# Kernel optimization log

Measured on AMD Instinct MI355X. Metric: run time of the kernel, lower is better.

The kernel has to match this reference:

```python
import jax, jax.numpy as jnp
import numpy as np

N = 100_000      # nodes
E = 1_600_000    # edges (avg degree 16)
IN = 512         # in_feats
HID = 4          # hidden_feats (forced equal to num_heads=4 by the mean(h,2) in forward)
H1 = 4           # heads in layer 1
OUT = 128        # out_feats
NEG_SLOPE = 0.2  # DGL GATConv leaky_relu default


def setup_inputs() -> dict:
    key = jax.random.key(0)
    ks = jax.random.split(key, 12)
    nfeats = jax.random.normal(ks[0], (N, IN), jnp.float32)
    efeats = jax.random.normal(ks[1], (E, 8), jnp.float32)  # unused by the module
    src = jax.random.randint(ks[2], (E,), 0, N, dtype=jnp.int32)
    dst = jax.random.randint(ks[3], (E,), 0, N, dtype=jnp.int32)
    # layer 1 params (in=IN, heads=H1, per-head out=HID)
    fc1_w = jax.random.normal(ks[4], (IN, H1 * HID), jnp.float32) / np.sqrt(IN)
    attn_l1 = jax.random.normal(ks[5], (H1, HID), jnp.float32) / np.sqrt(HID)
    attn_r1 = jax.random.normal(ks[6], (H1, HID), jnp.float32) / np.sqrt(HID)
    bias1 = jnp.zeros((H1 * HID,), jnp.float32)
    # layer 2 params (in=H1=4 after mean over feature dim, heads=1, out=OUT)
    fc2_w = jax.random.normal(ks[7], (HID, 1 * OUT), jnp.float32) / np.sqrt(HID)
    attn_l2 = jax.random.normal(ks[8], (1, OUT), jnp.float32) / np.sqrt(OUT)
    attn_r2 = jax.random.normal(ks[9], (1, OUT), jnp.float32) / np.sqrt(OUT)
    bias2 = jnp.zeros((OUT,), jnp.float32)
    return {"nfeats": nfeats, "efeats": efeats, "src": src, "dst": dst,
            "fc1_w": fc1_w, "attn_l1": attn_l1, "attn_r1": attn_r1, "bias1": bias1,
            "fc2_w": fc2_w, "attn_l2": attn_l2, "attn_r2": attn_r2, "bias2": bias2}


def gat_layer(x, src, dst, fc_w, attn_l, attn_r, bias, heads, d_out):
    # projection: (N, in) -> (N, H, D)
    h = (x @ fc_w).reshape(-1, heads, d_out)
    el = jnp.einsum('nhd,hd->nh', h, attn_l)   # (N, H)
    er = jnp.einsum('nhd,hd->nh', h, attn_r)
    e = jax.nn.leaky_relu(el[src] + er[dst], NEG_SLOPE)  # (E, H)
    # segment softmax over incoming edges of each dst node
    m = jax.lax.stop_gradient(jax.ops.segment_max(e, dst, num_segments=N))
    ex = jnp.exp(e - m[dst])
    denom = jax.ops.segment_sum(ex, dst, num_segments=N)
    alpha = ex / denom[dst]                    # (E, H)
    msg = alpha[:, :, None] * h[src]           # (E, H, D)
    rst = jax.ops.segment_sum(msg, dst, num_segments=N)  # (N, H, D)
    return rst + bias.reshape(1, heads, d_out)


def reference(nfeats, efeats, src, dst, fc1_w, attn_l1, attn_r1, bias1,
              fc2_w, attn_l2, attn_r2, bias2):
    h = gat_layer(nfeats, src, dst, fc1_w, attn_l1, attn_r1, bias1, H1, HID)  # (N,4,4)
    h = jnp.mean(h, axis=2)        # faithful to th.mean(h, 2): mean over per-head feat dim -> (N,4)
    h = jax.nn.relu(h)
    h = gat_layer(h, src, dst, fc2_w, attn_l2, attn_r2, bias2, 1, OUT)        # (N,1,OUT)
    return h.reshape(N, OUT)       # flatten(1)
```

## Files before the change

kernel.cpp:

```cpp
#include <hip/hip_runtime.h>
#include <math.h>

#define IN_F 512
#define OUTF 128
#define NEG_SLOPE 0.2f

typedef __attribute__((ext_vector_type(8))) short bf16x8;
typedef __attribute__((ext_vector_type(4))) float f32x4;

#define P1T 256
#define XP 136
#define NKS 16
#define BPSH 8192

#define NPB 128
#define NBMAX 784
#define EPB 4096
#define SRCMASK 0x1FFFF
#define CAP 2944

#define BP_BYTES (BPSH * 2)
#define XS_BYTES (4 * 16 * XP * 2)
#define SMEM_A   (BP_BYTES + XS_BYTES)

__device__ __forceinline__ unsigned pkbf(float a, float b) {
  unsigned ua = __float_as_uint(a); ua += 0x7FFF + ((ua >> 16) & 1);
  unsigned ub = __float_as_uint(b); ub += 0x7FFF + ((ub >> 16) & 1);
  return (ua >> 16) | (ub & 0xFFFF0000u);
}

__global__ void k_prep(const float* __restrict__ fc1, const float* __restrict__ al1,
                       const float* __restrict__ ar1, const float* __restrict__ fc2,
                       const float* __restrict__ al2, const float* __restrict__ ar2,
                       unsigned short* __restrict__ Bp,
                       float* __restrict__ w2al, float* __restrict__ w2ar,
                       int* __restrict__ bucketCursor) {
  __shared__ float wlds[IN_F * 12];
  int t = threadIdx.x;
  if (blockIdx.x == 0) {
    int k = t;
#pragma unroll
    for (int h = 0; h < 4; ++h) {
      float wl = 0.f, wr = 0.f, wb = 0.f;
#pragma unroll
      for (int j = 0; j < 4; ++j) {
        float wv = fc1[k * 16 + h * 4 + j];
        wl = fmaf(wv, al1[h * 4 + j], wl);
        wr = fmaf(wv, ar1[h * 4 + j], wr);
        wb += wv;
      }
      wlds[k * 12 + h] = wl;
      wlds[k * 12 + 4 + h] = wr;
      wlds[k * 12 + 8 + h] = 0.25f * wb;
    }
    __syncthreads();
    for (int item = t; item < NKS * 64; item += 512) {
      int s = item >> 6, l = item & 63;
      int col = l & 15;
      int kb = s * 32 + ((l >> 4) * 8);
      unsigned hi[4];
#pragma unroll
      for (int p = 0; p < 4; ++p) {
        float w0 = 0.f, w1 = 0.f;
        if (col < 12) {
          w0 = wlds[(kb + 2 * p) * 12 + col];
          w1 = wlds[(kb + 2 * p + 1) * 12 + col];
        }
        hi[p] = pkbf(w0, w1);
      }
      *(uint4*)&Bp[item * 8] = make_uint4(hi[0], hi[1], hi[2], hi[3]);
    }
  } else {
    if (t < 8) {
      int h = t >> 1;
      const float* a = (t & 1) ? ar2 : al2;
      float s = 0.f;
#pragma unroll 16
      for (int c = 0; c < OUTF; ++c) s += fc2[h * OUTF + c] * a[c];
      if (t & 1) w2ar[h] = s; else w2al[h] = s;
    }
    for (int i = t; i < NBMAX; i += 512) bucketCursor[i] = 0;
  }
}

__global__ __launch_bounds__(P1T) void k_A(
    const float* __restrict__ x, const unsigned short* __restrict__ Bp,
    float* __restrict__ pk1, float* __restrict__ er1, int n,
    const int* __restrict__ src, const int* __restrict__ dst,
    int* __restrict__ bucketCursor, unsigned* __restrict__ ep, int e,
    int projBlocks)
{
  __shared__ __align__(16) char smem[SMEM_A];
  const int t = threadIdx.x;

  if ((int)blockIdx.x < projBlocks) {
    const int lane = t & 63;
    const int wv = t >> 6;
    const bf16x8* Bfrag = (const bf16x8*)smem;
    short* xsw = (short*)(smem + BP_BYTES) + wv * (16 * XP);

    for (int i = t; i < NKS * 64; i += P1T)
      ((uint4*)smem)[i] = ((const uint4*)Bp)[i];
    __syncthreads();

    const int totalWaves = projBlocks * 4;
    const int rtMax = (n + 15) >> 4;
    for (int rt = blockIdx.x * 4 + wv; rt < rtMax; rt += totalWaves) {
      const int wrow = rt * 16;
      const float* __restrict__ xr = x + (size_t)wrow * IN_F;
      f32x4 acc = {0.f, 0.f, 0.f, 0.f};

      float4 st[8];
#pragma unroll
      for (int i = 0; i < 8; ++i) {
        int f = lane + i * 64;
        int r = f >> 5, c4 = (f & 31) * 4;
        st[i] = (wrow + r < n) ? *(const float4*)&xr[(size_t)r * IN_F + c4]
                               : make_float4(0.f, 0.f, 0.f, 0.f);
      }

      for (int kt = 0; kt < 4; ++kt) {
#pragma unroll
        for (int i = 0; i < 8; ++i) {
          int f = lane + i * 64;
          int r = f >> 5, c4 = (f & 31) * 4;
          uint2 pv; pv.x = pkbf(st[i].x, st[i].y); pv.y = pkbf(st[i].z, st[i].w);
          *(uint2*)&xsw[r * XP + c4] = pv;
        }
        if (kt < 3) {
          int kb = (kt + 1) * 128;
#pragma unroll
          for (int i = 0; i < 8; ++i) {
            int f = lane + i * 64;
            int r = f >> 5, c4 = (f & 31) * 4;
            st[i] = (wrow + r < n) ? *(const float4*)&xr[(size_t)r * IN_F + kb + c4]
                                   : make_float4(0.f, 0.f, 0.f, 0.f);
          }
        }
        asm volatile("s_waitcnt lgkmcnt(0)" ::: "memory");
        __builtin_amdgcn_sched_barrier(0);
#pragma unroll
        for (int ks = 0; ks < 4; ++ks) {
          bf16x8 a = *(const bf16x8*)&xsw[(lane & 15) * XP + ks * 32 + ((lane >> 4) * 8)];
          bf16x8 bh = Bfrag[(kt * 4 + ks) * 64 + lane];
          acc = __builtin_amdgcn_mfma_f32_16x16x32_bf16(a, bh, acc, 0, 0, 0);
        }
      }

      int col = lane & 15;
      int rbase = wrow + ((lane >> 4) * 4);
#pragma unroll
      for (int i = 0; i < 4; ++i) {
        int row = rbase + i;
        if (row < n) {
          float v = acc[i];
          if (col < 4)       pk1[(size_t)row * 8 + col] = v;
          else if (col < 8)  er1[(size_t)row * 4 + (col - 4)] = v;
          else if (col < 12) pk1[(size_t)row * 8 + 4 + (col - 8)] = v;
        }
      }
    }
  } else {
    int* hist = (int*)smem;
    int* base = hist + NBMAX;
    int* lcur = base + NBMAX;
    const int bb = blockIdx.x - projBlocks;
    for (int i = t; i < NBMAX; i += P1T) hist[i] = 0;
    __syncthreads();
    int blockBase = bb * EPB;
#pragma unroll
    for (int i = 0; i < EPB / P1T; ++i) {
      int idx = blockBase + t + i * P1T;
      if (idx < e) atomicAdd(&hist[dst[idx] >> 7], 1);
    }
    __syncthreads();
    for (int i = t; i < NBMAX; i += P1T) {
      if (hist[i] > 0) base[i] = atomicAdd(&bucketCursor[i], hist[i]);
      lcur[i] = 0;
    }
    __syncthreads();
#pragma unroll
    for (int i = 0; i < EPB / P1T; ++i) {
      int idx = blockBase + t + i * P1T;
      if (idx < e) {
        int d = dst[idx];
        int b = d >> 7;
        int off = base[b] + atomicAdd(&lcur[b], 1);
        if (off < CAP)
          ep[(size_t)b * CAP + off] = (unsigned)src[idx] | ((unsigned)(d & (NPB - 1)) << 17);
      }
    }
  }
}

__global__ __launch_bounds__(256) void k_B(
    const unsigned* __restrict__ ep, const int* __restrict__ bucketCursor,
    unsigned* __restrict__ ep2, int* __restrict__ nodeBeg, int* __restrict__ nodeEnd,
    const float* __restrict__ pk1, const float* __restrict__ er1,
    const float* __restrict__ bias1,
    const float* __restrict__ w2al, const float* __restrict__ w2ar,
    float* __restrict__ pk2, float* __restrict__ er2, int n)
{
  __shared__ int cnt[NPB];
  __shared__ int scn[NPB];
  __shared__ int cur[NPB];
  __shared__ unsigned lbuf[CAP];
  int t = threadIdx.x;
  int b = blockIdx.x;
  int nodeBase = b * NPB;
  int m = bucketCursor[b];
  if (m > CAP) m = CAP;
  const unsigned* __restrict__ in = ep + (size_t)b * CAP;
  if (t < NPB) cnt[t] = 0;
  __syncthreads();
  for (int j = t; j < m; j += 256) atomicAdd(&cnt[in[j] >> 17], 1);
  __syncthreads();
  if (t < NPB) scn[t] = cnt[t];
  __syncthreads();
  for (int off = 1; off < NPB; off <<= 1) {
    int v = (t < NPB && t >= off) ? scn[t - off] : 0;
    __syncthreads();
    if (t < NPB) scn[t] += v;
    __syncthreads();
  }
  if (t < NPB) {
    int excl = scn[t] - cnt[t];
    int node = nodeBase + t;
    if (node < n) {
      nodeBeg[node] = b * CAP + excl;
      nodeEnd[node] = b * CAP + excl + cnt[t];
    }
    cur[t] = excl;
  }
  __syncthreads();
  for (int j = t; j < m; j += 256) {
    unsigned p = in[j];
    int pos = atomicAdd(&cur[p >> 17], 1);
    lbuf[pos] = p & SRCMASK;
  }
  __syncthreads();
  for (int i = t; i < m; i += 256) ep2[(size_t)b * CAP + i] = lbuf[i];

#pragma unroll
  for (int half = 0; half < 2; ++half) {
    int w = t + half * 256;
    int i = w >> 2, h = w & 3;
    int node = nodeBase + i;
    bool active = node < n;
    float v = 0.f;
    if (active) {
      int beg = scn[i] - cnt[i], end = scn[i];
      float ern = er1[(size_t)node * 4 + h];
      float den = 0.f, num = 0.f;
      for (int j = beg; j < end; ++j) {
        int s = (int)lbuf[j];
        float el = pk1[(size_t)s * 8 + h];
        float hb = pk1[(size_t)s * 8 + 4 + h];
        float eh = el + ern;
        eh = (eh > 0.f) ? eh : NEG_SLOPE * eh;
        float wg = __expf(eh);
        den += wg;
        num = fmaf(wg, hb, num);
      }
      float mb = 0.25f * (bias1[h*4] + bias1[h*4+1] + bias1[h*4+2] + bias1[h*4+3]);
      v = (end > beg) ? num / den : 0.f;
      v += mb;
      v = (v > 0.f) ? v : 0.f;
    }
    float pl = v * w2al[h];
    float pr = v * w2ar[h];
    pl += __shfl_xor(pl, 1); pl += __shfl_xor(pl, 2);
    pr += __shfl_xor(pr, 1); pr += __shfl_xor(pr, 2);
    if (active) {
      pk2[(size_t)node * 8 + h] = v;
      if (h == 0) { pk2[(size_t)node * 8 + 4] = pl; er2[node] = pr; }
    }
  }
}

__global__ __launch_bounds__(256) void k_bagg2(
    const unsigned* __restrict__ ep2, const int* __restrict__ nodeBeg,
    const int* __restrict__ nodeEnd,
    const float* __restrict__ pk2, const float* __restrict__ er2,
    const float* __restrict__ w2, const float* __restrict__ bias2,
    float* __restrict__ out, int n)
{
  __shared__ float gacc[256 * 4];
  __shared__ float w2s[4 * OUTF];
  __shared__ float b2s[OUTF];
  int t = threadIdx.x;
  int nodeBase = blockIdx.x * 256;
  int nn = nodeBase + t;
  for (int i = t; i < 4 * OUTF; i += 256) w2s[i] = w2[i];
  if (t < OUTF) b2s[t] = bias2[t];
  float g0 = 0.f, g1 = 0.f, g2 = 0.f, g3 = 0.f;
  if (nn < n) {
    int beg = nodeBeg[nn], end = nodeEnd[nn];
    float ern = er2[nn];
    float den = 0.f;
    for (int j = beg; j < end; ++j) {
      int s = (int)ep2[j];
      const float* __restrict__ ps = &pk2[(size_t)s * 8];
      float4 hv = *(const float4*)ps;
      float e = ps[4] + ern;
      e = (e > 0.f) ? e : NEG_SLOPE * e;
      float w = __expf(e);
      den += w;
      g0 = fmaf(w, hv.x, g0); g1 = fmaf(w, hv.y, g1);
      g2 = fmaf(w, hv.z, g2); g3 = fmaf(w, hv.w, g3);
    }
    float inv = (end > beg) ? 1.0f / den : 0.f;
    g0 *= inv; g1 *= inv; g2 *= inv; g3 *= inv;
  }
  gacc[t * 4 + 0] = g0; gacc[t * 4 + 1] = g1;
  gacc[t * 4 + 2] = g2; gacc[t * 4 + 3] = g3;
  __syncthreads();
  for (int idx = t; idx < 256 * (OUTF / 2); idx += 256) {
    int i = idx >> 6;
    int node = nodeBase + i;
    if (node >= n) continue;
    int c = (idx & 63) * 2;
    float gx = gacc[i*4], gy = gacc[i*4+1], gz = gacc[i*4+2], gw = gacc[i*4+3];
    float2 o;
    o.x = gx*w2s[c]   + gy*w2s[OUTF+c]   + gz*w2s[2*OUTF+c]   + gw*w2s[3*OUTF+c]   + b2s[c];
    o.y = gx*w2s[c+1] + gy*w2s[OUTF+c+1] + gz*w2s[2*OUTF+c+1] + gw*w2s[3*OUTF+c+1] + b2s[c+1];
    *(float2*)&out[(size_t)node * OUTF + c] = o;
  }
}

extern "C" void kernel_launch(void* const* d_in, const int* in_sizes, int n_in,
                              void* d_out, int out_size, void* d_ws, size_t ws_size,
                              hipStream_t stream) {
  const float* nfeats = (const float*)d_in[0];
  const int*   srcp   = (const int*)d_in[2];
  const int*   dstp   = (const int*)d_in[3];
  const float* fc1    = (const float*)d_in[4];
  const float* al1    = (const float*)d_in[5];
  const float* ar1    = (const float*)d_in[6];
  const float* bias1  = (const float*)d_in[7];
  const float* fc2    = (const float*)d_in[8];
  const float* al2    = (const float*)d_in[9];
  const float* ar2    = (const float*)d_in[10];
  const float* bias2  = (const float*)d_in[11];

  const int N = in_sizes[0] / IN_F;
  const int E = in_sizes[2];
  const int NB = (N + NPB - 1) / NPB;

  float* ws   = (float*)d_ws;
  float* pk1  = ws;
  float* er1  = pk1 + (size_t)8 * N;
  float* pk2  = er1 + (size_t)4 * N;
  float* er2  = pk2 + (size_t)8 * N;
  float* w2al = er2 + N;
  float* w2ar = w2al + 4;
  unsigned short* Bp = (unsigned short*)(w2ar + 4);
  int* bucketCursor = (int*)(Bp + BPSH);
  int* nodeBeg      = bucketCursor + NBMAX;
  int* nodeEnd      = nodeBeg + N;
  unsigned* ep      = (unsigned*)(nodeEnd + N);
  unsigned* ep2     = ep + (size_t)NB * CAP;

  const int binBlocks = (E + EPB - 1) / EPB;
  const int projBlocks = 391;

  k_prep<<<2, 512, 0, stream>>>(fc1, al1, ar1, fc2, al2, ar2,
                                Bp, w2al, w2ar, bucketCursor);
  k_A<<<projBlocks + binBlocks, P1T, 0, stream>>>(nfeats, Bp, pk1, er1, N,
                                                  srcp, dstp, bucketCursor, ep, E,
                                                  projBlocks);
  k_B<<<NB, 256, 0, stream>>>(ep, bucketCursor, ep2, nodeBeg, nodeEnd,
                              pk1, er1, bias1, w2al, w2ar, pk2, er2, N);
  k_bagg2<<<(N + 255) / 256, 256, 0, stream>>>(ep2, nodeBeg, nodeEnd, pk2, er2,
                                               fc2, bias2, (float*)d_out, N);
}
```

Baseline: 136.6 us.

## Merge binning and projection into every block with dynamic tile scheduling

Kernel A used to give some blocks the projection and others the edge binning. Now every block first bins edges (if its index is below the binning block count) and then joins a work-stealing loop over 16-row projection tiles. Each wave grabs chunks of two tiles from a global atomic counter, which is reset in k_prep. Blocks grow to 512 threads and the grid is fixed at 768 blocks, with the aim of balancing load between the two phases and filling the GPU. The cost is global atomic contention and a doubled LDS footprint, which may cut occupancy.

Result: slower. 200.0 us (+46.4%).

```diff
diff --git a/kernel.cpp b/kernel.cpp
--- a/kernel.cpp
+++ b/kernel.cpp
@@ -8,10 +8,11 @@
 typedef __attribute__((ext_vector_type(8))) short bf16x8;
 typedef __attribute__((ext_vector_type(4))) float f32x4;
 
-#define P1T 256
+#define AT 512
 #define XP 136
 #define NKS 16
 #define BPSH 8192
+#define TCHUNK 2
 
 #define NPB 128
 #define NBMAX 784
@@ -20,7 +21,7 @@
 #define CAP 2944
 
 #define BP_BYTES (BPSH * 2)
-#define XS_BYTES (4 * 16 * XP * 2)
+#define XS_BYTES (8 * 16 * XP * 2)
 #define SMEM_A   (BP_BYTES + XS_BYTES)
 
 __device__ __forceinline__ unsigned pkbf(float a, float b) {
@@ -34,7 +35,7 @@
                        const float* __restrict__ al2, const float* __restrict__ ar2,
                        unsigned short* __restrict__ Bp,
                        float* __restrict__ w2al, float* __restrict__ w2ar,
-                       int* __restrict__ bucketCursor) {
+                       int* __restrict__ bucketCursor, int* __restrict__ tileCtr) {
   __shared__ float wlds[IN_F * 12];
   int t = threadIdx.x;
   if (blockIdx.x == 0) {
@@ -79,33 +80,70 @@
       for (int c = 0; c < OUTF; ++c) s += fc2[h * OUTF + c] * a[c];
       if (t & 1) w2ar[h] = s; else w2al[h] = s;
     }
+    if (t == 8) *tileCtr = 0;
     for (int i = t; i < NBMAX; i += 512) bucketCursor[i] = 0;
   }
 }
 
-__global__ __launch_bounds__(P1T) void k_A(
+__global__ __launch_bounds__(AT) void k_A(
     const float* __restrict__ x, const unsigned short* __restrict__ Bp,
     float* __restrict__ pk1, float* __restrict__ er1, int n,
     const int* __restrict__ src, const int* __restrict__ dst,
     int* __restrict__ bucketCursor, unsigned* __restrict__ ep, int e,
-    int projBlocks)
+    int* __restrict__ tileCtr, int bscatBlocks)
 {
   __shared__ __align__(16) char smem[SMEM_A];
   const int t = threadIdx.x;
 
-  if ((int)blockIdx.x < projBlocks) {
-    const int lane = t & 63;
-    const int wv = t >> 6;
-    const bf16x8* Bfrag = (const bf16x8*)smem;
-    short* xsw = (short*)(smem + BP_BYTES) + wv * (16 * XP);
-
-    for (int i = t; i < NKS * 64; i += P1T)
-      ((uint4*)smem)[i] = ((const uint4*)Bp)[i];
-    __syncthreads();
-
-    const int totalWaves = projBlocks * 4;
-    const int rtMax = (n + 15) >> 4;
-    for (int rt = blockIdx.x * 4 + wv; rt < rtMax; rt += totalWaves) {
+  if ((int)blockIdx.x < bscatBlocks) {
+    int* hist = (int*)smem;
+    int* base = hist + NBMAX;
+    int* lcur = base + NBMAX;
+    for (int i = t; i < NBMAX; i += AT) hist[i] = 0;
+    __syncthreads();
+    int blockBase = blockIdx.x * EPB;
+#pragma unroll
+    for (int i = 0; i < EPB / AT; ++i) {
+      int idx = blockBase + t + i * AT;
+      if (idx < e) atomicAdd(&hist[dst[idx] >> 7], 1);
+    }
+    __syncthreads();
+    for (int i = t; i < NBMAX; i += AT) {
+      if (hist[i] > 0) base[i] = atomicAdd(&bucketCursor[i], hist[i]);
+      lcur[i] = 0;
+    }
+    __syncthreads();
+#pragma unroll
+    for (int i = 0; i < EPB / AT; ++i) {
+      int idx = blockBase + t + i * AT;
+      if (idx < e) {
+        int d = dst[idx];
+        int b = d >> 7;
+        int off = base[b] + atomicAdd(&lcur[b], 1);
+        if (off < CAP)
+          ep[(size_t)b * CAP + off] = (unsigned)src[idx] | ((unsigned)(d & (NPB - 1)) << 17);
+      }
+    }
+    __syncthreads();
+  }
+
+  const int lane = t & 63;
+  const int wv = t >> 6;
+  const bf16x8* Bfrag = (const bf16x8*)smem;
+  short* xsw = (short*)(smem + BP_BYTES) + wv * (16 * XP);
+
+  for (int i = t; i < NKS * 64; i += AT)
+    ((uint4*)smem)[i] = ((const uint4*)Bp)[i];
+  __syncthreads();
+
+  const int rtMax = (n + 15) >> 4;
+  for (;;) {
+    int rt0;
+    if (lane == 0) rt0 = atomicAdd(tileCtr, TCHUNK);
+    rt0 = __shfl(rt0, 0);
+    if (rt0 >= rtMax) break;
+    int rtEnd = (rt0 + TCHUNK < rtMax) ? rt0 + TCHUNK : rtMax;
+    for (int rt = rt0; rt < rtEnd; ++rt) {
       const int wrow = rt * 16;
       const float* __restrict__ xr = x + (size_t)wrow * IN_F;
       f32x4 acc = {0.f, 0.f, 0.f, 0.f};
@@ -158,36 +196,6 @@
           else if (col < 8)  er1[(size_t)row * 4 + (col - 4)] = v;
           else if (col < 12) pk1[(size_t)row * 8 + 4 + (col - 8)] = v;
         }
-      }
-    }
-  } else {
-    int* hist = (int*)smem;
-    int* base = hist + NBMAX;
-    int* lcur = base + NBMAX;
-    const int bb = blockIdx.x - projBlocks;
-    for (int i = t; i < NBMAX; i += P1T) hist[i] = 0;
-    __syncthreads();
-    int blockBase = bb * EPB;
-#pragma unroll
-    for (int i = 0; i < EPB / P1T; ++i) {
-      int idx = blockBase + t + i * P1T;
-      if (idx < e) atomicAdd(&hist[dst[idx] >> 7], 1);
-    }
-    __syncthreads();
-    for (int i = t; i < NBMAX; i += P1T) {
-      if (hist[i] > 0) base[i] = atomicAdd(&bucketCursor[i], hist[i]);
-      lcur[i] = 0;
-    }
-    __syncthreads();
-#pragma unroll
-    for (int i = 0; i < EPB / P1T; ++i) {
-      int idx = blockBase + t + i * P1T;
-      if (idx < e) {
-        int d = dst[idx];
-        int b = d >> 7;
-        int off = base[b] + atomicAdd(&lcur[b], 1);
-        if (off < CAP)
-          ep[(size_t)b * CAP + off] = (unsigned)src[idx] | ((unsigned)(d & (NPB - 1)) << 17);
       }
     }
   }
@@ -356,19 +364,20 @@
   float* w2ar = w2al + 4;
   unsigned short* Bp = (unsigned short*)(w2ar + 4);
   int* bucketCursor = (int*)(Bp + BPSH);
-  int* nodeBeg      = bucketCursor + NBMAX;
+  int* tileCtr      = bucketCursor + NBMAX;
+  int* nodeBeg      = tileCtr + 1;
   int* nodeEnd      = nodeBeg + N;
   unsigned* ep      = (unsigned*)(nodeEnd + N);
   unsigned* ep2     = ep + (size_t)NB * CAP;
 
-  const int binBlocks = (E + EPB - 1) / EPB;
-  const int projBlocks = 391;
+  const int bscatBlocks = (E + EPB - 1) / EPB;
+  const int aBlocks = 768;
 
   k_prep<<<2, 512, 0, stream>>>(fc1, al1, ar1, fc2, al2, ar2,
-                                Bp, w2al, w2ar, bucketCursor);
-  k_A<<<projBlocks + binBlocks, P1T, 0, stream>>>(nfeats, Bp, pk1, er1, N,
-                                                  srcp, dstp, bucketCursor, ep, E,
-                                                  projBlocks);
+                                Bp, w2al, w2ar, bucketCursor, tileCtr);
+  k_A<<<aBlocks, AT, 0, stream>>>(nfeats, Bp, pk1, er1, N,
+                                  srcp, dstp, bucketCursor, ep, E,
+                                  tileCtr, bscatBlocks);
   k_B<<<NB, 256, 0, stream>>>(ep, bucketCursor, ep2, nodeBeg, nodeEnd,
                               pk1, er1, bias1, w2al, w2ar, pk2, er2, N);
   k_bagg2<<<(N + 255) / 256, 256, 0, stream>>>(ep2, nodeBeg, nodeEnd, pk2, er2,
```
